# Kernel tuning notes

Measured on AMD Instinct MI355X. Metric: run time of the kernel, lower is better.

The kernel has to match this reference:

```python
import jax, jax.numpy as jnp
import numpy as np

DIM = 768
NUM_HEADS = 12
HEAD_DIM = DIM // NUM_HEADS
SCALE = HEAD_DIM ** -0.5


def setup_inputs() -> dict:
    key = jax.random.key(0)
    k_x, k_qkv, k_proj, k_pb = jax.random.split(key, 4)
    B, N, C = 16, 1024, DIM
    x = jax.random.normal(k_x, (B, N, C), dtype=jnp.float32)
    # qkv Linear: weight [3C, C], no bias (qkv_bias=False)
    w_qkv = jax.random.normal(k_qkv, (3 * C, C), dtype=jnp.float32) * (C ** -0.5)
    # proj Linear: weight [C, C], bias [C]
    w_proj = jax.random.normal(k_proj, (C, C), dtype=jnp.float32) * (C ** -0.5)
    b_proj = jax.random.normal(k_pb, (C,), dtype=jnp.float32) * 0.01
    return {"x": x, "w_qkv": w_qkv, "w_proj": w_proj, "b_proj": b_proj}


def reference(x, w_qkv, w_proj, b_proj):
    B, N, C = x.shape
    H, D = NUM_HEADS, HEAD_DIM
    # qkv projection: [B,N,3C] -> [3,B,H,N,D]
    qkv = jnp.einsum('bnc,ec->bne', x, w_qkv)
    qkv = qkv.reshape(B, N, 3, H, D).transpose(2, 0, 3, 1, 4)
    q, k, v = qkv[0], qkv[1], qkv[2]
    # manual attention: scores [B,H,N,N] materialized, as in source
    attn = jnp.einsum('bhqd,bhkd->bhqk', q, k) * SCALE
    attn = jax.nn.softmax(attn, axis=-1)
    out = jnp.einsum('bhqk,bhkd->bhqd', attn, v)  # [B,H,N,D]
    out = out.transpose(0, 2, 1, 3).reshape(B, N, C)
    out = jnp.einsum('bnc,oc->bno', out, w_proj) + b_proj
    return out
```

## Files before the change

kernel.cpp:

```cpp
#include <hip/hip_runtime.h>
#include <hip/hip_bf16.h>
#include <stdint.h>

typedef __attribute__((ext_vector_type(8))) short short8;
typedef __attribute__((ext_vector_type(4))) short short4v;
typedef __attribute__((ext_vector_type(4))) float floatx4;

#define B_   16
#define N_   1024
#define C_   768
#define H_   12
#define D_   64
#define K_   768
#define QSCALE 0.18033688011112042f

__device__ __forceinline__ short f2bf(float f) {
    __hip_bfloat16 h = __float2bfloat16(f);
    short s; __builtin_memcpy(&s, &h, 2); return s;
}

__device__ __forceinline__ void gl_lds16(const void* g, void* l) {
    __builtin_amdgcn_global_load_lds(
        (const __attribute__((address_space(1))) unsigned int*)g,
        (__attribute__((address_space(3))) unsigned int*)l, 16, 0, 0);
}

__global__ void cvt_bf16(const float* __restrict__ in, short* __restrict__ out, int n8)
{
    const int i = blockIdx.x * 256 + threadIdx.x;
    if (i >= n8) return;
    const float4* p = (const float4*)in + 2 * (long)i;
    const float4 u = p[0], v = p[1];
    short8 r;
    r[0] = f2bf(u.x); r[1] = f2bf(u.y); r[2] = f2bf(u.z); r[3] = f2bf(u.w);
    r[4] = f2bf(v.x); r[5] = f2bf(v.y); r[6] = f2bf(v.z); r[7] = f2bf(v.w);
    *((short8*)out + i) = r;
}

template<int MODE>
__global__ __launch_bounds__(256, 2)
void gemm_bt(const short* __restrict__ A, const short* __restrict__ Bm,
             const float* __restrict__ bias,
             short* __restrict__ q_ws, short* __restrict__ k_ws,
             short* __restrict__ v_ws, float* __restrict__ outp)
{
    __shared__ short Alds[128 * 32];
    __shared__ short Blds[128 * 32];
    const int tid  = threadIdx.x;
    const int wave = tid >> 6, lane = tid & 63;
    const int cl   = lane & 15, quad = lane >> 4;
    const int bm = blockIdx.x, bn = blockIdx.y;
    const int wm = (wave >> 1) * 64, wn = (wave & 1) * 64;

    const short* Ag = A  + (long)bm * 128 * K_ + (long)(tid >> 2) * K_ + (tid & 3) * 8;
    const short* Bg = Bm + (long)bn * 128 * K_ + (long)(tid >> 2) * K_ + (tid & 3) * 8;
    short* la = Alds + (tid & 0xC0) * 8;
    short* lb = Blds + (tid & 0xC0) * 8;

    const floatx4 fzero = {0.f, 0.f, 0.f, 0.f};
    floatx4 acc[4][4];
    #pragma unroll
    for (int i = 0; i < 4; i++)
        #pragma unroll
        for (int j = 0; j < 4; j++) acc[i][j] = fzero;

    for (int kt = 0; kt < K_; kt += 32) {
        __syncthreads();
        gl_lds16(Ag + kt,            la);
        gl_lds16(Ag + kt + 64 * K_,  la + 2048);
        gl_lds16(Bg + kt,            lb);
        gl_lds16(Bg + kt + 64 * K_,  lb + 2048);
        __syncthreads();

        short8 af[4], bf[4];
        #pragma unroll
        for (int i = 0; i < 4; i++)
            af[i] = *(const short8*)(Alds + (wm + i * 16 + cl) * 32 + quad * 8);
        #pragma unroll
        for (int j = 0; j < 4; j++)
            bf[j] = *(const short8*)(Blds + (wn + j * 16 + cl) * 32 + quad * 8);
        #pragma unroll
        for (int i = 0; i < 4; i++)
            #pragma unroll
            for (int j = 0; j < 4; j++)
                acc[i][j] = __builtin_amdgcn_mfma_f32_16x16x32_bf16(af[i], bf[j], acc[i][j], 0, 0, 0);
    }

    #pragma unroll
    for (int i = 0; i < 4; i++) {
        const int gm0 = bm * 128 + wm + i * 16 + quad * 4;
        #pragma unroll
        for (int j = 0; j < 4; j++) {
            const int gn = bn * 128 + wn + j * 16 + cl;
            if (MODE == 0) {
                const int t   = bn / 6;
                const int rem = gn - t * 768;
                const int h   = rem >> 6, d = rem & 63;
                const int b   = gm0 >> 10;
                const int n0  = gm0 & 1023;
                const int bh  = b * H_ + h;
                if (t == 2) {
                    short4v pk;
                    #pragma unroll
                    for (int r = 0; r < 4; r++) pk[r] = f2bf(acc[i][j][r]);
                    *(short4v*)(v_ws + (((long)(bh * D_ + d)) << 10) + n0) = pk;
                } else {
                    short* dst = (t == 0) ? q_ws : k_ws;
                    const float sc = (t == 0) ? QSCALE : 1.0f;
                    #pragma unroll
                    for (int r = 0; r < 4; r++)
                        dst[((long)bh * N_ + (n0 + r)) * D_ + d] = f2bf(acc[i][j][r] * sc);
                }
            } else {
                const float bv = bias[gn];
                #pragma unroll
                for (int r = 0; r < 4; r++)
                    outp[(long)(gm0 + r) * C_ + gn] = acc[i][j][r] + bv;
            }
        }
    }
}

__global__ __launch_bounds__(256, 2)
void attn_fused(const short* __restrict__ q_ws, const short* __restrict__ k_ws,
                const short* __restrict__ v_ws, short* __restrict__ o_ws)
{
    __shared__ short Klds[128 * 72];
    __shared__ short Vlds[64 * 136];
    __shared__ short Plds[4][16 * 136];

    const int tid  = threadIdx.x;
    const int wave = tid >> 6, lane = tid & 63;
    const int cl   = lane & 15, quad = lane >> 4;

    const int linear = blockIdx.y * 8 + blockIdx.x;
    const int xcd = linear & 7, slot = linear >> 3;
    const int bh  = xcd * 24 + (slot >> 3);
    const int qt  = slot & 7;

    const long base = (long)bh * (N_ * D_);
    const int  qr0  = qt * 128 + wave * 32 + cl;

    short8 qf[2][2];
    #pragma unroll
    for (int mt = 0; mt < 2; mt++) {
        qf[mt][0] = *(const short8*)(q_ws + base + (long)(qr0 + mt * 16) * D_ + quad * 8);
        qf[mt][1] = *(const short8*)(q_ws + base + (long)(qr0 + mt * 16) * D_ + 32 + quad * 8);
    }

    const floatx4 fzero = {0.f, 0.f, 0.f, 0.f};
    float m_r[2][4], l_r[2][4];
    floatx4 o_acc[2][4];
    #pragma unroll
    for (int mt = 0; mt < 2; mt++)
        #pragma unroll
        for (int r = 0; r < 4; r++) {
            m_r[mt][r] = -1e30f; l_r[mt][r] = 0.f; o_acc[mt][r] = fzero;
        }

    const int skey = tid >> 3, sseg = (tid & 7) * 8;
    const int vd   = tid >> 4, vseg = (tid & 15) * 8;
    short* pl = &Plds[wave][0];

    for (int kc = 0; kc < N_; kc += 128) {
        short8 kst[4], vst[4];
        #pragma unroll
        for (int p = 0; p < 4; p++) {
            kst[p] = *(const short8*)(k_ws + base + (long)(kc + p * 32 + skey) * D_ + sseg);
            vst[p] = *(const short8*)(v_ws + base + (long)(p * 16 + vd) * N_ + kc + vseg);
        }
        __syncthreads();
        #pragma unroll
        for (int p = 0; p < 4; p++) {
            *(short8*)(Klds + (p * 32 + skey) * 72 + sseg) = kst[p];
            *(short8*)(Vlds + (p * 16 + vd) * 136 + vseg)  = vst[p];
        }
        __syncthreads();

        #pragma unroll
        for (int mt = 0; mt < 2; mt++) {
            floatx4 s[8];
            #pragma unroll
            for (int nt = 0; nt < 8; nt++) {
                short8 kf0 = *(const short8*)(Klds + (nt * 16 + cl) * 72 + quad * 8);
                short8 kf1 = *(const short8*)(Klds + (nt * 16 + cl) * 72 + 32 + quad * 8);
                floatx4 t4 = fzero;
                t4 = __builtin_amdgcn_mfma_f32_16x16x32_bf16(qf[mt][0], kf0, t4, 0, 0, 0);
                t4 = __builtin_amdgcn_mfma_f32_16x16x32_bf16(qf[mt][1], kf1, t4, 0, 0, 0);
                s[nt] = t4;
            }

            float alpha[4];
            #pragma unroll
            for (int r = 0; r < 4; r++) {
                float v = s[0][r];
                #pragma unroll
                for (int nt = 1; nt < 8; nt++) v = fmaxf(v, s[nt][r]);
                v = fmaxf(v, __shfl_xor(v, 1));
                v = fmaxf(v, __shfl_xor(v, 2));
                v = fmaxf(v, __shfl_xor(v, 4));
                v = fmaxf(v, __shfl_xor(v, 8));
                const float mn = fmaxf(m_r[mt][r], v);
                alpha[r] = __builtin_amdgcn_exp2f(m_r[mt][r] - mn);
                m_r[mt][r] = mn;
                l_r[mt][r] *= alpha[r];
            }
            #pragma unroll
            for (int nt = 0; nt < 8; nt++) {
                #pragma unroll
                for (int r = 0; r < 4; r++) {
                    const float p = __builtin_amdgcn_exp2f(s[nt][r] - m_r[mt][r]);
                    l_r[mt][r] += p;
                    pl[(quad * 4 + r) * 136 + nt * 16 + cl] = f2bf(p);
                }
            }
            #pragma unroll
            for (int dt = 0; dt < 4; dt++) {
                o_acc[mt][dt][0] *= alpha[0]; o_acc[mt][dt][1] *= alpha[1];
                o_acc[mt][dt][2] *= alpha[2]; o_acc[mt][dt][3] *= alpha[3];
            }
            asm volatile("" ::: "memory");

            #pragma unroll
            for (int ks = 0; ks < 4; ks++) {
                short8 pf = *(const short8*)(pl + cl * 136 + ks * 32 + quad * 8);
                #pragma unroll
                for (int dt = 0; dt < 4; dt++) {
                    short8 vf = *(const short8*)(Vlds + (dt * 16 + cl) * 136 + ks * 32 + quad * 8);
                    o_acc[mt][dt] = __builtin_amdgcn_mfma_f32_16x16x32_bf16(pf, vf, o_acc[mt][dt], 0, 0, 0);
                }
            }
            asm volatile("" ::: "memory");
        }
    }

    const int b = bh / H_, h = bh - b * H_;
    #pragma unroll
    for (int mt = 0; mt < 2; mt++) {
        #pragma unroll
        for (int r = 0; r < 4; r++) {
            float v = l_r[mt][r];
            v += __shfl_xor(v, 1); v += __shfl_xor(v, 2);
            v += __shfl_xor(v, 4); v += __shfl_xor(v, 8);
            l_r[mt][r] = 1.0f / v;
        }
        const int nrow = qt * 128 + wave * 32 + mt * 16 + quad * 4;
        #pragma unroll
        for (int dt = 0; dt < 4; dt++) {
            const int c = h * D_ + dt * 16 + cl;
            #pragma unroll
            for (int r = 0; r < 4; r++)
                o_ws[((long)(b * N_ + nrow + r)) * C_ + c] = f2bf(o_acc[mt][dt][r] * l_r[mt][r]);
        }
    }
}

extern "C" void kernel_launch(void* const* d_in, const int* in_sizes, int n_in,
                              void* d_out, int out_size, void* d_ws, size_t ws_size,
                              hipStream_t stream)
{
    const float* x      = (const float*)d_in[0];
    const float* w_qkv  = (const float*)d_in[1];
    const float* w_proj = (const float*)d_in[2];
    const float* b_proj = (const float*)d_in[3];
    float* out = (float*)d_out;

    const long SZ = (long)B_ * N_ * C_;
    short* q_ws   = (short*)d_ws;
    short* k_ws   = q_ws + SZ;
    short* v_ws   = k_ws + SZ;
    short* x_bf   = v_ws + SZ;
    short* o_ws   = x_bf;
    short* wqkv_bf  = x_bf + SZ;
    short* wproj_bf = wqkv_bf + (long)3 * C_ * C_;

    cvt_bf16<<<dim3(6144), 256, 0, stream>>>(x,      x_bf,     (int)(SZ / 8));
    cvt_bf16<<<dim3(864),  256, 0, stream>>>(w_qkv,  wqkv_bf,  3 * C_ * C_ / 8);
    cvt_bf16<<<dim3(288),  256, 0, stream>>>(w_proj, wproj_bf, C_ * C_ / 8);

    gemm_bt<0><<<dim3(128, 18), 256, 0, stream>>>(x_bf, wqkv_bf, nullptr, q_ws, k_ws, v_ws, nullptr);
    attn_fused<<<dim3(8, 192), 256, 0, stream>>>(q_ws, k_ws, v_ws, o_ws);
    gemm_bt<1><<<dim3(128, 6), 256, 0, stream>>>(o_ws, wproj_bf, b_proj, nullptr, nullptr, nullptr, out);
}
```

Baseline: 321.6 us.

## Merge conversion kernels, raise occupancy bounds, vectorize P stores with permuted key order

Merges the three fp32-to-bf16 conversion launches into one kernel. Raises launch bounds to three blocks per CU for the GEMM and attention kernels. In attention, the softmax probabilities are packed as bf16 pairs and written to LDS as one 16-byte store per row. To keep P·V correct under the new key column order, V is loaded with a matching strided permutation. The V global loads become eight scalar 2-byte loads per thread instead of one vector load, and the tighter register budget may cause spills.

```diff
diff --git a/kernel.cpp b/kernel.cpp
--- a/kernel.cpp
+++ b/kernel.cpp
@@ -18,6 +18,10 @@
     __hip_bfloat16 h = __float2bfloat16(f);
     short s; __builtin_memcpy(&s, &h, 2); return s;
 }
+__device__ __forceinline__ unsigned pk2bf(float a, float b) {
+    __hip_bfloat162 h = __float22bfloat162_rn(make_float2(a, b));
+    unsigned u; __builtin_memcpy(&u, &h, 4); return u;
+}
 
 __device__ __forceinline__ void gl_lds16(const void* g, void* l) {
     __builtin_amdgcn_global_load_lds(
@@ -25,20 +29,28 @@
         (__attribute__((address_space(3))) unsigned int*)l, 16, 0, 0);
 }
 
-__global__ void cvt_bf16(const float* __restrict__ in, short* __restrict__ out, int n8)
+#define N8_X  1572864
+#define N8_WQ 221184
+#define N8_WP 73728
+__global__ void cvt_all(const float* __restrict__ x, const float* __restrict__ wq,
+                        const float* __restrict__ wp, short* __restrict__ xb,
+                        short* __restrict__ wqb, short* __restrict__ wpb)
 {
-    const int i = blockIdx.x * 256 + threadIdx.x;
-    if (i >= n8) return;
-    const float4* p = (const float4*)in + 2 * (long)i;
+    long i = (long)blockIdx.x * 256 + threadIdx.x;
+    const float* src; short* dst;
+    if (i < N8_X)              { src = x;  dst = xb;  }
+    else if (i < N8_X + N8_WQ) { src = wq; dst = wqb; i -= N8_X; }
+    else                       { src = wp; dst = wpb; i -= (long)N8_X + N8_WQ; }
+    const float4* p = (const float4*)src + 2 * i;
     const float4 u = p[0], v = p[1];
     short8 r;
     r[0] = f2bf(u.x); r[1] = f2bf(u.y); r[2] = f2bf(u.z); r[3] = f2bf(u.w);
     r[4] = f2bf(v.x); r[5] = f2bf(v.y); r[6] = f2bf(v.z); r[7] = f2bf(v.w);
-    *((short8*)out + i) = r;
+    *((short8*)dst + i) = r;
 }
 
 template<int MODE>
-__global__ __launch_bounds__(256, 2)
+__global__ __launch_bounds__(256, 3)
 void gemm_bt(const short* __restrict__ A, const short* __restrict__ Bm,
              const float* __restrict__ bias,
              short* __restrict__ q_ws, short* __restrict__ k_ws,
@@ -121,7 +133,7 @@
     }
 }
 
-__global__ __launch_bounds__(256, 2)
+__global__ __launch_bounds__(256, 3)
 void attn_fused(const short* __restrict__ q_ws, const short* __restrict__ k_ws,
                 const short* __restrict__ v_ws, short* __restrict__ o_ws)
 {
@@ -159,7 +171,7 @@
         }
 
     const int skey = tid >> 3, sseg = (tid & 7) * 8;
-    const int vd   = tid >> 4, vseg = (tid & 15) * 8;
+    const int vd   = tid >> 4, vc = tid & 15;
     short* pl = &Plds[wave][0];
 
     for (int kc = 0; kc < N_; kc += 128) {
@@ -167,13 +179,15 @@
         #pragma unroll
         for (int p = 0; p < 4; p++) {
             kst[p] = *(const short8*)(k_ws + base + (long)(kc + p * 32 + skey) * D_ + sseg);
-            vst[p] = *(const short8*)(v_ws + base + (long)(p * 16 + vd) * N_ + kc + vseg);
+            #pragma unroll
+            for (int i = 0; i < 8; i++)
+                vst[p][i] = v_ws[base + (long)(p * 16 + vd) * N_ + kc + i * 16 + vc];
         }
         __syncthreads();
         #pragma unroll
         for (int p = 0; p < 4; p++) {
             *(short8*)(Klds + (p * 32 + skey) * 72 + sseg) = kst[p];
-            *(short8*)(Vlds + (p * 16 + vd) * 136 + vseg)  = vst[p];
+            *(short8*)(Vlds + (p * 16 + vd) * 136 + vc * 8) = vst[p];
         }
         __syncthreads();
 
@@ -206,13 +220,18 @@
                 l_r[mt][r] *= alpha[r];
             }
             #pragma unroll
-            for (int nt = 0; nt < 8; nt++) {
-                #pragma unroll
-                for (int r = 0; r < 4; r++) {
-                    const float p = __builtin_amdgcn_exp2f(s[nt][r] - m_r[mt][r]);
-                    l_r[mt][r] += p;
-                    pl[(quad * 4 + r) * 136 + nt * 16 + cl] = f2bf(p);
-                }
+            for (int r = 0; r < 4; r++) {
+                float p0 = __builtin_amdgcn_exp2f(s[0][r] - m_r[mt][r]);
+                float p1 = __builtin_amdgcn_exp2f(s[1][r] - m_r[mt][r]);
+                float p2 = __builtin_amdgcn_exp2f(s[2][r] - m_r[mt][r]);
+                float p3 = __builtin_amdgcn_exp2f(s[3][r] - m_r[mt][r]);
+                float p4 = __builtin_amdgcn_exp2f(s[4][r] - m_r[mt][r]);
+                float p5 = __builtin_amdgcn_exp2f(s[5][r] - m_r[mt][r]);
+                float p6 = __builtin_amdgcn_exp2f(s[6][r] - m_r[mt][r]);
+                float p7 = __builtin_amdgcn_exp2f(s[7][r] - m_r[mt][r]);
+                l_r[mt][r] += ((p0 + p1) + (p2 + p3)) + ((p4 + p5) + (p6 + p7));
+                uint4 pk = { pk2bf(p0, p1), pk2bf(p2, p3), pk2bf(p4, p5), pk2bf(p6, p7) };
+                *(uint4*)(pl + (quad * 4 + r) * 136 + cl * 8) = pk;
             }
             #pragma unroll
             for (int dt = 0; dt < 4; dt++) {
@@ -274,10 +293,7 @@
     short* wqkv_bf  = x_bf + SZ;
     short* wproj_bf = wqkv_bf + (long)3 * C_ * C_;
 
-    cvt_bf16<<<dim3(6144), 256, 0, stream>>>(x,      x_bf,     (int)(SZ / 8));
-    cvt_bf16<<<dim3(864),  256, 0, stream>>>(w_qkv,  wqkv_bf,  3 * C_ * C_ / 8);
-    cvt_bf16<<<dim3(288),  256, 0, stream>>>(w_proj, wproj_bf, C_ * C_ / 8);
-
+    cvt_all<<<dim3(7296), 256, 0, stream>>>(x, w_qkv, w_proj, x_bf, wqkv_bf, wproj_bf);
     gemm_bt<0><<<dim3(128, 18), 256, 0, stream>>>(x_bf, wqkv_bf, nullptr, q_ws, k_ws, v_ws, nullptr);
     attn_fused<<<dim3(8, 192), 256, 0, stream>>>(q_ws, k_ws, v_ws, o_ws);
     gemm_bt<1><<<dim3(128, 6), 256, 0, stream>>>(o_ws, wproj_bf, b_proj, nullptr, nullptr, nullptr, out);
```

Result: faster. 313.2 us (-2.6%).
